# Kernel optimization log

Measured on AMD Instinct MI355X. Metric: run time of the kernel, lower is better.

The kernel has to match this reference:

```python
import jax, jax.numpy as jnp
import numpy as np

N_NODES = 100000
EPS = 1e-5


def gcn_conv(x, edge_index, W, b):
    # PyG GCNConv: add self loops, symmetric normalization, aggregate at target.
    n = x.shape[0]
    xw = x @ W                                  # [N, F_out]
    loop = jnp.arange(n)
    src = jnp.concatenate([edge_index[0], loop])
    dst = jnp.concatenate([edge_index[1], loop])
    deg = jax.ops.segment_sum(jnp.ones_like(dst, dtype=xw.dtype), dst, num_segments=n)
    dinv = jnp.where(deg > 0, jax.lax.rsqrt(deg), 0.0)
    norm = dinv[src] * dinv[dst]                # [E+N]
    out = jax.ops.segment_sum(norm[:, None] * xw[src], dst, num_segments=n)
    return out + b


def batch_norm(x, gamma, beta):
    # training-mode BatchNorm1d over node dim
    m = x.mean(axis=0)
    v = x.var(axis=0)
    return (x - m) * jax.lax.rsqrt(v + EPS) * gamma + beta


def setup_inputs() -> dict:
    key = jax.random.key(0)
    ks = jax.random.split(key, 16)
    dims = [(128, 256), (256, 128), (128, 64)]
    inp = {
        "x": jax.random.normal(ks[0], (N_NODES, 128), dtype=jnp.float32),
        "edge_index": jax.random.randint(ks[1], (2, 1600000), 0, N_NODES),
        "pos_edge_index": jax.random.randint(ks[2], (2, 200000), 0, N_NODES),
        "neg_edge_index": jax.random.randint(ks[3], (2, 200000), 0, N_NODES),
    }
    for i, (fi, fo) in enumerate(dims, start=1):
        inp[f"W{i}"] = jax.random.normal(ks[3 + i], (fi, fo), dtype=jnp.float32) / np.sqrt(fi)
        inp[f"b{i}"] = jnp.zeros((fo,), dtype=jnp.float32)
        inp[f"g{i}"] = jnp.ones((fo,), dtype=jnp.float32)
        inp[f"beta{i}"] = jnp.zeros((fo,), dtype=jnp.float32)
    return inp


def reference(x, edge_index, pos_edge_index, neg_edge_index,
              W1, b1, g1, beta1, W2, b2, g2, beta2, W3, b3, g3, beta3):
    # encode
    h = gcn_conv(x, edge_index, W1, b1)
    h = jax.nn.sigmoid(batch_norm(h, g1, beta1))
    h = gcn_conv(h, edge_index, W2, b2)
    h = jax.nn.sigmoid(batch_norm(h, g2, beta2))
    h = gcn_conv(h, edge_index, W3, b3)
    z = batch_norm(h, g3, beta3)                # [N, 64]
    # decode
    ei = jnp.concatenate([pos_edge_index, neg_edge_index], axis=-1)
    logits = jnp.sum(z[ei[0]] * z[ei[1]], axis=-1)
    return logits
```

## Files before the change

### kernel.cpp

```cpp
#include <hip/hip_runtime.h>
#include <hip/hip_bf16.h>
#include <stddef.h>


#define WAVE 64
#define BSHIFT 9
#define SCHUNK 4096

typedef __attribute__((ext_vector_type(8))) short short8;
typedef __attribute__((ext_vector_type(4))) float f32x4;

__device__ __forceinline__ float bl(uint g) { return __uint_as_float(g << 16); }
__device__ __forceinline__ float bh(uint g) { return __uint_as_float(g & 0xffff0000u); }
__device__ __forceinline__ ushort f2b(float f) {
    uint u = __float_as_uint(f);
    return (ushort)((u + 0x7fffu + ((u >> 16) & 1u)) >> 16);
}
__device__ __forceinline__ uint pack2(float lo, float hi) {
    return (uint)f2b(lo) | ((uint)f2b(hi) << 16);
}

__device__ __forceinline__ void gload16(const ushort* g, ushort* l) {
    __builtin_amdgcn_global_load_lds(
        (const __attribute__((address_space(1))) uint*)g,
        (__attribute__((address_space(3))) uint*)l, 16, 0, 0);
}

__global__ __launch_bounds__(256) void k_bhist(const int* __restrict__ dst, int* __restrict__ gh, int E) {
    __shared__ int lh[256];
    lh[threadIdx.x] = 0; __syncthreads();
    int i = blockIdx.x * 256 + threadIdx.x, stride = gridDim.x * 256;
    for (; i < E; i += stride) atomicAdd(&lh[dst[i] >> BSHIFT], 1);
    __syncthreads();
    int v = lh[threadIdx.x];
    if (v) atomicAdd(&gh[threadIdx.x], v);
}

__global__ void k_bscan(const int* __restrict__ gh, int* __restrict__ boff, int* __restrict__ bcur) {
    __shared__ int ls[256];
    int t = threadIdx.x;
    int v = gh[t];
    ls[t] = v; __syncthreads();
    for (int off = 1; off < 256; off <<= 1) {
        int x = (t >= off) ? ls[t - off] : 0;
        __syncthreads();
        ls[t] += x;
        __syncthreads();
    }
    int excl = ls[t] - v;
    boff[t] = excl; bcur[t] = excl;
    if (t == 255) boff[256] = ls[255];
}

__global__ __launch_bounds__(256) void k_bscatter(const int* __restrict__ src, const int* __restrict__ dst,
                                                  int* __restrict__ gcur, uint* __restrict__ pairs, int E) {
    __shared__ int lh[256];
    int t = threadIdx.x;
    int base = blockIdx.x * SCHUNK;
    lh[t] = 0; __syncthreads();
    int rs[16], rd[16];
    #pragma unroll
    for (int i = 0; i < 16; ++i) {
        int idx = base + i * 256 + t;
        if (idx < E) { rs[i] = src[idx]; rd[i] = dst[idx]; atomicAdd(&lh[rd[i] >> BSHIFT], 1); }
        else rd[i] = -1;
    }
    __syncthreads();
    int cnt_b = lh[t];
    int b0 = cnt_b ? atomicAdd(&gcur[t], cnt_b) : 0;
    lh[t] = b0;
    __syncthreads();
    #pragma unroll
    for (int i = 0; i < 16; ++i) {
        if (rd[i] >= 0) {
            int p = atomicAdd(&lh[rd[i] >> BSHIFT], 1);
            pairs[p] = ((uint)(rd[i] & 511) << 17) | (uint)rs[i];
        }
    }
}

__global__ __launch_bounds__(256) void k_bfine(const uint* __restrict__ pairs, const int* __restrict__ boff,
                                               int* __restrict__ rowptr, int* __restrict__ srcs,
                                               float* __restrict__ dinv, int N, int E) {
    __shared__ int lcnt[512];
    __shared__ int ls[256];
    int b = blockIdx.x, t = threadIdx.x;
    int d0 = b << BSHIFT;
    int e0 = boff[b], e1 = boff[b + 1];
    lcnt[t] = 0; lcnt[t + 256] = 0;
    __syncthreads();
    for (int e = e0 + t; e < e1; e += 256)
        atomicAdd(&lcnt[pairs[e] >> 17], 1);
    __syncthreads();
    int c0 = lcnt[2 * t], c1 = lcnt[2 * t + 1];
    ls[t] = c0 + c1;
    __syncthreads();
    for (int off = 1; off < 256; off <<= 1) {
        int x = (t >= off) ? ls[t - off] : 0;
        __syncthreads();
        ls[t] += x;
        __syncthreads();
    }
    int excl = ls[t] - (c0 + c1);
    int s0 = excl, s1 = excl + c0;
    int d = d0 + 2 * t;
    if (d < N)     { rowptr[d] = e0 + s0;     dinv[d] = rsqrtf((float)(c0 + 1)); }
    if (d + 1 < N) { rowptr[d + 1] = e0 + s1; dinv[d + 1] = rsqrtf((float)(c1 + 1)); }
    if (b == 0 && t == 0) rowptr[N] = E;
    lcnt[2 * t] = s0; lcnt[2 * t + 1] = s1;
    __syncthreads();
    for (int e = e0 + t; e < e1; e += 256) {
        uint p = pairs[e];
        int pos = atomicAdd(&lcnt[p >> 17], 1);
        srcs[e0 + pos] = (int)(p & 0x1FFFFu);
    }
}

__global__ void k_convx(const float* __restrict__ in, ushort* __restrict__ out, size_t n4) {
    size_t i = (size_t)blockIdx.x * blockDim.x + threadIdx.x;
    if (i >= n4) return;
    float4 v = reinterpret_cast<const float4*>(in)[i];
    uint2 o;
    o.x = pack2(v.x, v.y);
    o.y = pack2(v.z, v.w);
    reinterpret_cast<uint2*>(out)[i] = o;
}

__global__ void k_convW(const float* __restrict__ W1, const float* __restrict__ W2,
                        const float* __restrict__ W3, ushort* __restrict__ Wt1,
                        ushort* __restrict__ Wt2, ushort* __restrict__ Wt3) {
    int i = blockIdx.x * blockDim.x + threadIdx.x;
    const float* W; ushort* Wt; int K, Nn, j;
    if (i < 32768)      { W = W1; Wt = Wt1; K = 128; Nn = 256; j = i; }
    else if (i < 65536) { W = W2; Wt = Wt2; K = 256; Nn = 128; j = i - 32768; }
    else if (i < 73728) { W = W3; Wt = Wt3; K = 128; Nn = 64;  j = i - 65536; }
    else return;
    int k = j / Nn, n = j % Nn;
    Wt[(size_t)n * K + k] = f2b(W[k * Nn + n]);
}

template<int F>
__global__ __launch_bounds__(256) void k_agg(const ushort* __restrict__ in, ushort* __restrict__ out,
                                             const int* __restrict__ rowptr, const int* __restrict__ srcs,
                                             const float* __restrict__ dinv, int N) {
    constexpr int L = (F * 2) / 16;
    int wv = threadIdx.x >> 6, lane = threadIdx.x & 63;
    int node = (blockIdx.x * 4 + wv) * (64 / L) + lane / L;
    int sl = lane % L;
    if (node >= N) return;
    const uint4* inq = reinterpret_cast<const uint4*>(in);
    float di = dinv[node];
    float acc[8];
    {
        uint4 v = inq[(size_t)node * L + sl];
        acc[0] = di * bl(v.x); acc[1] = di * bh(v.x);
        acc[2] = di * bl(v.y); acc[3] = di * bh(v.y);
        acc[4] = di * bl(v.z); acc[5] = di * bh(v.z);
        acc[6] = di * bl(v.w); acc[7] = di * bh(v.w);
    }
    int e = rowptr[node], e1 = rowptr[node + 1];
    for (; e + 3 < e1; e += 4) {
        int s0 = srcs[e], s1 = srcs[e + 1], s2 = srcs[e + 2], s3 = srcs[e + 3];
        float d0 = dinv[s0], d1 = dinv[s1], d2 = dinv[s2], d3 = dinv[s3];
        uint4 v0 = inq[(size_t)s0 * L + sl];
        uint4 v1 = inq[(size_t)s1 * L + sl];
        uint4 v2 = inq[(size_t)s2 * L + sl];
        uint4 v3 = inq[(size_t)s3 * L + sl];
        acc[0] += d0 * bl(v0.x) + d1 * bl(v1.x) + d2 * bl(v2.x) + d3 * bl(v3.x);
        acc[1] += d0 * bh(v0.x) + d1 * bh(v1.x) + d2 * bh(v2.x) + d3 * bh(v3.x);
        acc[2] += d0 * bl(v0.y) + d1 * bl(v1.y) + d2 * bl(v2.y) + d3 * bl(v3.y);
        acc[3] += d0 * bh(v0.y) + d1 * bh(v1.y) + d2 * bh(v2.y) + d3 * bh(v3.y);
        acc[4] += d0 * bl(v0.z) + d1 * bl(v1.z) + d2 * bl(v2.z) + d3 * bl(v3.z);
        acc[5] += d0 * bh(v0.z) + d1 * bh(v1.z) + d2 * bh(v2.z) + d3 * bh(v3.z);
        acc[6] += d0 * bl(v0.w) + d1 * bl(v1.w) + d2 * bl(v2.w) + d3 * bl(v3.w);
        acc[7] += d0 * bh(v0.w) + d1 * bh(v1.w) + d2 * bh(v2.w) + d3 * bh(v3.w);
    }
    for (; e < e1; ++e) {
        int s0 = srcs[e];
        float d0 = dinv[s0];
        uint4 v0 = inq[(size_t)s0 * L + sl];
        acc[0] += d0 * bl(v0.x); acc[1] += d0 * bh(v0.x);
        acc[2] += d0 * bl(v0.y); acc[3] += d0 * bh(v0.y);
        acc[4] += d0 * bl(v0.z); acc[5] += d0 * bh(v0.z);
        acc[6] += d0 * bl(v0.w); acc[7] += d0 * bh(v0.w);
    }
    uint4 o;
    o.x = pack2(acc[0] * di, acc[1] * di);
    o.y = pack2(acc[2] * di, acc[3] * di);
    o.z = pack2(acc[4] * di, acc[5] * di);
    o.w = pack2(acc[6] * di, acc[7] * di);
    reinterpret_cast<uint4*>(out)[(size_t)node * L + sl] = o;
}

template<int F>
__global__ __launch_bounds__(256) void k_bnstats(const ushort* __restrict__ h, float* __restrict__ gsum,
                                                 float* __restrict__ gsq, int N) {
    constexpr int C = F / 8;
    constexpr int RPW = 64 / C;
    __shared__ float ls[4][16][16];
    int wv = threadIdx.x >> 6, lane = threadIdx.x & 63;
    int fidx = lane % C, rsub = lane / C;
    int row = (blockIdx.x * 4 + wv) * RPW + rsub;
    int rstride = gridDim.x * 4 * RPW;
    const uint4* hq = reinterpret_cast<const uint4*>(h);
    float s[8] = {}, q[8] = {};
    for (int r = row; r < N; r += rstride) {
        uint4 v = hq[(size_t)r * C + fidx];
        float x;
        x = bl(v.x); s[0] += x; q[0] += x * x;
        x = bh(v.x); s[1] += x; q[1] += x * x;
        x = bl(v.y); s[2] += x; q[2] += x * x;
        x = bh(v.y); s[3] += x; q[3] += x * x;
        x = bl(v.z); s[4] += x; q[4] += x * x;
        x = bh(v.z); s[5] += x; q[5] += x * x;
        x = bl(v.w); s[6] += x; q[6] += x * x;
        x = bh(v.w); s[7] += x; q[7] += x * x;
    }
    #pragma unroll
    for (int m = C; m < 64; m <<= 1) {
        #pragma unroll
        for (int j = 0; j < 8; ++j) { s[j] += __shfl_xor(s[j], m); q[j] += __shfl_xor(q[j], m); }
    }
    if (lane < C) {
        #pragma unroll
        for (int j = 0; j < 8; ++j) { ls[wv][lane][j] = s[j]; ls[wv][lane][8 + j] = q[j]; }
    }
    __syncthreads();
    int t = threadIdx.x;
    if (t < F) {
        int ch = t / 8, j = t % 8;
        float S = 0.f, Q = 0.f;
        #pragma unroll
        for (int w = 0; w < 4; ++w) { S += ls[w][ch][j]; Q += ls[w][ch][8 + j]; }
        atomicAdd(&gsum[t], S); atomicAdd(&gsq[t], Q);
    }
}

template<int F>
__global__ __launch_bounds__(256) void k_apply(ushort* __restrict__ h,
                                               const float* __restrict__ bsum, const float* __restrict__ bsq,
                                               const float* __restrict__ bg, const float* __restrict__ bb,
                                               float invN, long NT) {
    constexpr int CPR = F / 8;
    int tid = blockIdx.x * 256 + threadIdx.x;
    int fb = (tid % CPR) * 8;
    float sc[8], sh[8];
    #pragma unroll
    for (int j = 0; j < 8; ++j) {
        float m = bsum[fb + j] * invN;
        float var = bsq[fb + j] * invN - m * m;
        float s = bg[fb + j] * rsqrtf(var + 1e-5f);
        sc[j] = s; sh[j] = bb[fb + j] - m * s;
    }
    uint4* hq = reinterpret_cast<uint4*>(h);
    long stride = (long)gridDim.x * 256;
    for (long i = tid; i < NT; i += stride) {
        uint4 v = hq[i];
        float x[8];
        x[0] = bl(v.x); x[1] = bh(v.x); x[2] = bl(v.y); x[3] = bh(v.y);
        x[4] = bl(v.z); x[5] = bh(v.z); x[6] = bl(v.w); x[7] = bh(v.w);
        #pragma unroll
        for (int j = 0; j < 8; ++j) {
            float y = x[j] * sc[j] + sh[j];
            x[j] = 1.f / (1.f + __expf(-y));
        }
        v.x = pack2(x[0], x[1]); v.y = pack2(x[2], x[3]);
        v.z = pack2(x[4], x[5]); v.w = pack2(x[6], x[7]);
        hq[i] = v;
    }
}

template<int K, int NF, int NPASS, bool STATS>
__global__ __launch_bounds__(256) void k_gemm(const ushort* __restrict__ A, const ushort* __restrict__ Wt,
                                              ushort* __restrict__ C, int M, int Nout,
                                              float* __restrict__ gsum, float* __restrict__ gsq) {
    constexpr int S = K / 64;
    constexpr int KS = K / 32;
    __shared__ ushort Alds[2][128 * 64];
    int m0 = blockIdx.x * 128;
    int t = threadIdx.x;
    int w = t >> 6, lane = t & 63;
    int wr = w >> 1, wc = w & 1;
    int rf = lane & 15, kg = lane >> 4;

    auto stage = [&](int buf, int step) {
        #pragma unroll
        for (int i = 0; i < 4; ++i) {
            int cb = (i * 4 + w) * 64;
            int chunk = cb + lane;
            int r = chunk >> 3, cs = chunk & 7;
            int c = cs ^ (r & 7);
            int gr = m0 + r; if (gr >= M) gr = M - 1;
            gload16(A + (size_t)gr * K + step * 64 + c * 8, &Alds[buf][cb * 8]);
        }
    };

    for (int pass = 0; pass < NPASS; ++pass) {
        int n0 = pass * NF * 32;
        const ushort* bp[NF];
        #pragma unroll
        for (int nf = 0; nf < NF; ++nf)
            bp[nf] = Wt + (size_t)(n0 + wc * (NF * 16) + nf * 16 + rf) * K + kg * 8;

        f32x4 acc[4][NF];
        #pragma unroll
        for (int mf = 0; mf < 4; ++mf)
            #pragma unroll
            for (int nf = 0; nf < NF; ++nf)
                acc[mf][nf] = (f32x4){0.f, 0.f, 0.f, 0.f};

        if (pass == 0) {
            stage(0, 0);
            if constexpr (S == 2) stage(1, 1);
            __syncthreads();
        }

        short8 bcur[NF];
        #pragma unroll
        for (int nf = 0; nf < NF; ++nf)
            bcur[nf] = *reinterpret_cast<const short8*>(bp[nf]);

        for (int s = 0; s < S; ++s) {
            if constexpr (S > 2) {
                if (s + 1 < S && pass == 0) stage((s + 1) & 1, s + 1);
            }
            #pragma unroll
            for (int ksl = 0; ksl < 2; ++ksl) {
                int gs = s * 2 + ksl;
                short8 bnxt[NF];
                if (gs + 1 < KS) {
                    #pragma unroll
                    for (int nf = 0; nf < NF; ++nf)
                        bnxt[nf] = *reinterpret_cast<const short8*>(bp[nf] + (gs + 1) * 32);
                }
                short8 a[4];
                #pragma unroll
                for (int mf = 0; mf < 4; ++mf) {
                    int R = wr * 64 + mf * 16 + rf;
                    int idx = R * 8 + ((ksl * 4 + kg) ^ (R & 7));
                    a[mf] = *reinterpret_cast<const short8*>(&Alds[s & 1][idx * 8]);
                }
                #pragma unroll
                for (int mf = 0; mf < 4; ++mf)
                    #pragma unroll
                    for (int nf = 0; nf < NF; ++nf)
                        acc[mf][nf] = __builtin_amdgcn_mfma_f32_16x16x32_bf16(a[mf], bcur[nf], acc[mf][nf], 0, 0, 0);
                if (gs + 1 < KS) {
                    #pragma unroll
                    for (int nf = 0; nf < NF; ++nf) bcur[nf] = bnxt[nf];
                }
            }
            if constexpr (S > 2) __syncthreads();
        }

        #pragma unroll
        for (int mf = 0; mf < 4; ++mf)
            #pragma unroll
            for (int nf = 0; nf < NF; ++nf) {
                int col = n0 + wc * (NF * 16) + nf * 16 + rf;
                #pragma unroll
                for (int j = 0; j < 4; ++j) {
                    int row = m0 + wr * 64 + mf * 16 + kg * 4 + j;
                    if (row < M) C[(size_t)row * Nout + col] = f2b(acc[mf][nf][j]);
                }
            }

        if constexpr (STATS) {
            __shared__ float bns[2][NF * 32], bnq[2][NF * 32];
            __syncthreads();
            #pragma unroll
            for (int nf = 0; nf < NF; ++nf) {
                float cs = 0.f, cq = 0.f;
                #pragma unroll
                for (int mf = 0; mf < 4; ++mf)
                    #pragma unroll
                    for (int j = 0; j < 4; ++j) {
                        int row = m0 + wr * 64 + mf * 16 + kg * 4 + j;
                        float v = (row < M) ? acc[mf][nf][j] : 0.f;
                        cs += v; cq += v * v;
                    }
                cs += __shfl_xor(cs, 16); cs += __shfl_xor(cs, 32);
                cq += __shfl_xor(cq, 16); cq += __shfl_xor(cq, 32);
                if (kg == 0) { bns[wr][wc * (NF * 16) + nf * 16 + rf] = cs; bnq[wr][wc * (NF * 16) + nf * 16 + rf] = cq; }
            }
            __syncthreads();
            if (t < NF * 32) {
                atomicAdd(&gsum[n0 + t], bns[0][t] + bns[1][t]);
                atomicAdd(&gsq[n0 + t],  bnq[0][t] + bnq[1][t]);
            }
        }
    }
}

__global__ __launch_bounds__(256) void k_decode(const ushort* __restrict__ h,
                                                const float* __restrict__ bsum, const float* __restrict__ bsq,
                                                const float* __restrict__ bg, const float* __restrict__ bb,
                                                float invN,
                                                const int* __restrict__ pos, const int* __restrict__ neg,
                                                int Pp, int Pn, float* __restrict__ out) {
    __shared__ float scl[64], shl[64];
    int t = threadIdx.x;
    if (t < 64) {
        float m = bsum[t] * invN;
        float var = bsq[t] * invN - m * m;
        float sc = bg[t] * rsqrtf(var + 1e-5f);
        scl[t] = sc; shl[t] = bb[t] - m * sc;
    }
    __syncthreads();
    int gid = blockIdx.x * 16 + (t >> 4);
    int l = t & 15;
    int P = Pp + Pn;
    if (gid >= P) return;
    int a, b;
    if (gid < Pp) { a = pos[gid]; b = pos[Pp + gid]; }
    else          { int e = gid - Pp; a = neg[e]; b = neg[Pn + e]; }
    const uint2* hu = reinterpret_cast<const uint2*>(h);
    uint2 ua = hu[(size_t)a * 16 + l];
    uint2 ub = hu[(size_t)b * 16 + l];
    int f = l * 4;
    float s0 = scl[f], s1 = scl[f + 1], s2 = scl[f + 2], s3 = scl[f + 3];
    float t0 = shl[f], t1 = shl[f + 1], t2 = shl[f + 2], t3 = shl[f + 3];
    float a0 = bl(ua.x) * s0 + t0, a1 = bh(ua.x) * s1 + t1, a2 = bl(ua.y) * s2 + t2, a3 = bh(ua.y) * s3 + t3;
    float b0 = bl(ub.x) * s0 + t0, b1 = bh(ub.x) * s1 + t1, b2 = bl(ub.y) * s2 + t2, b3 = bh(ub.y) * s3 + t3;
    float d = a0 * b0 + a1 * b1 + a2 * b2 + a3 * b3;
    d += __shfl_xor(d, 1);
    d += __shfl_xor(d, 2);
    d += __shfl_xor(d, 4);
    d += __shfl_xor(d, 8);
    if (l == 0) out[gid] = d;
}

extern "C" void kernel_launch(void* const* d_in, const int* in_sizes, int n_in,
                              void* d_out, int out_size, void* d_ws, size_t ws_size,
                              hipStream_t stream) {
    const float* x   = (const float*)d_in[0];
    const int*   ei  = (const int*)d_in[1];
    const int*   pe  = (const int*)d_in[2];
    const int*   ne  = (const int*)d_in[3];
    const float* W1  = (const float*)d_in[4];
    const float* g1  = (const float*)d_in[6];
    const float* be1 = (const float*)d_in[7];
    const float* W2  = (const float*)d_in[8];
    const float* g2  = (const float*)d_in[10];
    const float* be2 = (const float*)d_in[11];
    const float* W3  = (const float*)d_in[12];
    const float* g3  = (const float*)d_in[14];
    const float* be3 = (const float*)d_in[15];
    float* out = (float*)d_out;

    const int N  = in_sizes[0] / 128;
    const int E  = in_sizes[1] / 2;
    const int Pp = in_sizes[2] / 2;
    const int Pn = in_sizes[3] / 2;
    const float invN = 1.0f / (float)N;

    char* ws = (char*)d_ws;
    auto carve = [&](size_t bytes) -> char* {
        char* p = ws;
        ws += (bytes + 255) & ~(size_t)255;
        return p;
    };
    char*  zz     = carve(256 * 4 + 896 * 4);
    int*   gh     = (int*)zz;
    float* sums1  = (float*)(zz + 1024);
    float* sq1    = sums1 + 256;
    float* sums2  = sq1 + 256;
    float* sq2    = sums2 + 128;
    float* sums3  = sq2 + 128;
    float* sq3    = sums3 + 64;
    size_t zz_bytes = 1024 + 896 * 4;

    int*    boff   = (int*)carve(257 * 4);
    int*    bcur   = (int*)carve(256 * 4);
    int*    rowptr = (int*)carve((size_t)(N + 1) * 4);
    float*  dinv   = (float*)carve((size_t)N * 4);
    int*    srcs   = (int*)carve((size_t)E * 4);
    uint*   pairs  = (uint*)carve((size_t)E * 4);
    ushort* Wt1    = (ushort*)carve(128 * 256 * 2);
    ushort* Wt2    = (ushort*)carve(256 * 128 * 2);
    ushort* Wt3    = (ushort*)carve(128 * 64 * 2);
    ushort* b1     = (ushort*)carve((size_t)N * 128 * 2);
    ushort* b2     = (ushort*)carve((size_t)N * 128 * 2);
    ushort* b3     = (ushort*)carve((size_t)N * 256 * 2);

    const int* e_src = ei;
    const int* e_dst = ei + E;
    const int NBUCK = (N + (1 << BSHIFT) - 1) >> BSHIFT;

    hipMemsetAsync(zz, 0, zz_bytes, stream);

    k_bhist<<<2048, 256, 0, stream>>>(e_dst, gh, E);
    k_bscan<<<1, 256, 0, stream>>>(gh, boff, bcur);
    k_bscatter<<<(E + SCHUNK - 1) / SCHUNK, 256, 0, stream>>>(e_src, e_dst, bcur, pairs, E);
    k_bfine<<<NBUCK, 256, 0, stream>>>(pairs, boff, rowptr, srcs, dinv, N, E);

    {
        size_t n4 = (size_t)N * 128 / 4;
        k_convx<<<(int)((n4 + 255) / 256), 256, 0, stream>>>(x, b1, n4);
        k_convW<<<288, 256, 0, stream>>>(W1, W2, W3, Wt1, Wt2, Wt3);
    }

    const int mblk = (N + 127) / 128;
    const int agg128 = (N + 15) / 16;
    const int agg64  = (N + 31) / 32;

    k_agg<128><<<agg128, 256, 0, stream>>>(b1, b2, rowptr, srcs, dinv, N);
    k_gemm<128, 4, 2, true><<<mblk, 256, 0, stream>>>(b2, Wt1, b3, N, 256, sums1, sq1);
    k_apply<256><<<2048, 256, 0, stream>>>(b3, sums1, sq1, g1, be1, invN, (long)N * 32);

    k_gemm<256, 4, 1, false><<<mblk, 256, 0, stream>>>(b3, Wt2, b1, N, 128, nullptr, nullptr);
    k_agg<128><<<agg128, 256, 0, stream>>>(b1, b2, rowptr, srcs, dinv, N);
    k_bnstats<128><<<512, 256, 0, stream>>>(b2, sums2, sq2, N);
    k_apply<128><<<2048, 256, 0, stream>>>(b2, sums2, sq2, g2, be2, invN, (long)N * 16);

    k_gemm<128, 2, 1, false><<<mblk, 256, 0, stream>>>(b2, Wt3, b1, N, 64, nullptr, nullptr);
    k_agg<64><<<agg64, 256, 0, stream>>>(b1, b2, rowptr, srcs, dinv, N);
    k_bnstats<64><<<512, 256, 0, stream>>>(b2, sums3, sq3, N);

    k_decode<<<(Pp + Pn + 15) / 16, 256, 0, stream>>>(b2, sums3, sq3, g3, be3, invN,
                                                      pe, ne, Pp, Pn, out);
}
```

Baseline: 544.4 us.

## Prescale features by source dinv to drop per-edge dinv gathers in aggregation

The source-side normalization dinv[src] is moved out of the aggregation loop. The input features are pre-multiplied by dinv once per node, in the x conversion kernel and in the GEMM epilogues for layers 2 and 3. The aggregation kernel then sums raw neighbor rows with no per-edge dinv gather or multiply, and its main loop is unrolled to 8 loads in flight. The W and x conversion kernels are merged into one launch. The cost is an extra rounding step: the features are scaled before they are stored as bf16.

```diff
diff --git a/kernel.cpp b/kernel.cpp
--- a/kernel.cpp
+++ b/kernel.cpp
@@ -116,27 +116,29 @@
     }
 }
 
-__global__ void k_convx(const float* __restrict__ in, ushort* __restrict__ out, size_t n4) {
-    size_t i = (size_t)blockIdx.x * blockDim.x + threadIdx.x;
-    if (i >= n4) return;
-    float4 v = reinterpret_cast<const float4*>(in)[i];
+__global__ void k_conv(const float* __restrict__ W1, const float* __restrict__ W2,
+                       const float* __restrict__ W3, ushort* __restrict__ Wt1,
+                       ushort* __restrict__ Wt2, ushort* __restrict__ Wt3,
+                       const float* __restrict__ x, const float* __restrict__ dinv,
+                       ushort* __restrict__ xs, size_t n4) {
+    size_t i = (size_t)blockIdx.x * 256 + threadIdx.x;
+    if (i < 73728) {
+        const float* W; ushort* Wt; int K, Nn; size_t j;
+        if (i < 32768)      { W = W1; Wt = Wt1; K = 128; Nn = 256; j = i; }
+        else if (i < 65536) { W = W2; Wt = Wt2; K = 256; Nn = 128; j = i - 32768; }
+        else                { W = W3; Wt = Wt3; K = 128; Nn = 64;  j = i - 65536; }
+        int k = (int)(j / Nn), n = (int)(j % Nn);
+        Wt[(size_t)n * K + k] = f2b(W[(size_t)k * Nn + n]);
+        return;
+    }
+    size_t j = i - 73728;
+    if (j >= n4) return;
+    float d = dinv[j / 32];
+    float4 v = reinterpret_cast<const float4*>(x)[j];
     uint2 o;
-    o.x = pack2(v.x, v.y);
-    o.y = pack2(v.z, v.w);
-    reinterpret_cast<uint2*>(out)[i] = o;
-}
-
-__global__ void k_convW(const float* __restrict__ W1, const float* __restrict__ W2,
-                        const float* __restrict__ W3, ushort* __restrict__ Wt1,
-                        ushort* __restrict__ Wt2, ushort* __restrict__ Wt3) {
-    int i = blockIdx.x * blockDim.x + threadIdx.x;
-    const float* W; ushort* Wt; int K, Nn, j;
-    if (i < 32768)      { W = W1; Wt = Wt1; K = 128; Nn = 256; j = i; }
-    else if (i < 65536) { W = W2; Wt = Wt2; K = 256; Nn = 128; j = i - 32768; }
-    else if (i < 73728) { W = W3; Wt = Wt3; K = 128; Nn = 64;  j = i - 65536; }
-    else return;
-    int k = j / Nn, n = j % Nn;
-    Wt[(size_t)n * K + k] = f2b(W[k * Nn + n]);
+    o.x = pack2(d * v.x, d * v.y);
+    o.y = pack2(d * v.z, d * v.w);
+    reinterpret_cast<uint2*>(xs)[j] = o;
 }
 
 template<int F>
@@ -153,36 +155,48 @@
     float acc[8];
     {
         uint4 v = inq[(size_t)node * L + sl];
-        acc[0] = di * bl(v.x); acc[1] = di * bh(v.x);
-        acc[2] = di * bl(v.y); acc[3] = di * bh(v.y);
-        acc[4] = di * bl(v.z); acc[5] = di * bh(v.z);
-        acc[6] = di * bl(v.w); acc[7] = di * bh(v.w);
+        acc[0] = bl(v.x); acc[1] = bh(v.x);
+        acc[2] = bl(v.y); acc[3] = bh(v.y);
+        acc[4] = bl(v.z); acc[5] = bh(v.z);
+        acc[6] = bl(v.w); acc[7] = bh(v.w);
     }
     int e = rowptr[node], e1 = rowptr[node + 1];
+    for (; e + 7 < e1; e += 8) {
+        int s[8];
+        #pragma unroll
+        for (int i = 0; i < 8; ++i) s[i] = srcs[e + i];
+        uint4 v[8];
+        #pragma unroll
+        for (int i = 0; i < 8; ++i) v[i] = inq[(size_t)s[i] * L + sl];
+        #pragma unroll
+        for (int i = 0; i < 8; ++i) {
+            acc[0] += bl(v[i].x); acc[1] += bh(v[i].x);
+            acc[2] += bl(v[i].y); acc[3] += bh(v[i].y);
+            acc[4] += bl(v[i].z); acc[5] += bh(v[i].z);
+            acc[6] += bl(v[i].w); acc[7] += bh(v[i].w);
+        }
+    }
     for (; e + 3 < e1; e += 4) {
-        int s0 = srcs[e], s1 = srcs[e + 1], s2 = srcs[e + 2], s3 = srcs[e + 3];
-        float d0 = dinv[s0], d1 = dinv[s1], d2 = dinv[s2], d3 = dinv[s3];
-        uint4 v0 = inq[(size_t)s0 * L + sl];
-        uint4 v1 = inq[(size_t)s1 * L + sl];
-        uint4 v2 = inq[(size_t)s2 * L + sl];
-        uint4 v3 = inq[(size_t)s3 * L + sl];
-        acc[0] += d0 * bl(v0.x) + d1 * bl(v1.x) + d2 * bl(v2.x) + d3 * bl(v3.x);
-        acc[1] += d0 * bh(v0.x) + d1 * bh(v1.x) + d2 * bh(v2.x) + d3 * bh(v3.x);
-        acc[2] += d0 * bl(v0.y) + d1 * bl(v1.y) + d2 * bl(v2.y) + d3 * bl(v3.y);
-        acc[3] += d0 * bh(v0.y) + d1 * bh(v1.y) + d2 * bh(v2.y) + d3 * bh(v3.y);
-        acc[4] += d0 * bl(v0.z) + d1 * bl(v1.z) + d2 * bl(v2.z) + d3 * bl(v3.z);
-        acc[5] += d0 * bh(v0.z) + d1 * bh(v1.z) + d2 * bh(v2.z) + d3 * bh(v3.z);
-        acc[6] += d0 * bl(v0.w) + d1 * bl(v1.w) + d2 * bl(v2.w) + d3 * bl(v3.w);
-        acc[7] += d0 * bh(v0.w) + d1 * bh(v1.w) + d2 * bh(v2.w) + d3 * bh(v3.w);
+        int s[4];
+        #pragma unroll
+        for (int i = 0; i < 4; ++i) s[i] = srcs[e + i];
+        uint4 v[4];
+        #pragma unroll
+        for (int i = 0; i < 4; ++i) v[i] = inq[(size_t)s[i] * L + sl];
+        #pragma unroll
+        for (int i = 0; i < 4; ++i) {
+            acc[0] += bl(v[i].x); acc[1] += bh(v[i].x);
+            acc[2] += bl(v[i].y); acc[3] += bh(v[i].y);
+            acc[4] += bl(v[i].z); acc[5] += bh(v[i].z);
+            acc[6] += bl(v[i].w); acc[7] += bh(v[i].w);
+        }
     }
     for (; e < e1; ++e) {
-        int s0 = srcs[e];
-        float d0 = dinv[s0];
-        uint4 v0 = inq[(size_t)s0 * L + sl];
-        acc[0] += d0 * bl(v0.x); acc[1] += d0 * bh(v0.x);
-        acc[2] += d0 * bl(v0.y); acc[3] += d0 * bh(v0.y);
-        acc[4] += d0 * bl(v0.z); acc[5] += d0 * bh(v0.z);
-        acc[6] += d0 * bl(v0.w); acc[7] += d0 * bh(v0.w);
+        uint4 v0 = inq[(size_t)srcs[e] * L + sl];
+        acc[0] += bl(v0.x); acc[1] += bh(v0.x);
+        acc[2] += bl(v0.y); acc[3] += bh(v0.y);
+        acc[4] += bl(v0.z); acc[5] += bh(v0.z);
+        acc[6] += bl(v0.w); acc[7] += bh(v0.w);
     }
     uint4 o;
     o.x = pack2(acc[0] * di, acc[1] * di);
@@ -270,9 +284,10 @@
     }
 }
 
-template<int K, int NF, int NPASS, bool STATS>
+template<int K, int NF, int NPASS, bool STATS, bool PRESCALE>
 __global__ __launch_bounds__(256) void k_gemm(const ushort* __restrict__ A, const ushort* __restrict__ Wt,
                                               ushort* __restrict__ C, int M, int Nout,
+                                              const float* __restrict__ dinv,
                                               float* __restrict__ gsum, float* __restrict__ gsq) {
     constexpr int S = K / 64;
     constexpr int KS = K / 32;
@@ -294,6 +309,17 @@
             gload16(A + (size_t)gr * K + step * 64 + c * 8, &Alds[buf][cb * 8]);
         }
     };
+
+    float dreg[4][4];
+    if constexpr (PRESCALE) {
+        #pragma unroll
+        for (int mf = 0; mf < 4; ++mf)
+            #pragma unroll
+            for (int j = 0; j < 4; ++j) {
+                int row = m0 + wr * 64 + mf * 16 + kg * 4 + j;
+                dreg[mf][j] = (row < M) ? dinv[row] : 0.f;
+            }
+    }
 
     for (int pass = 0; pass < NPASS; ++pass) {
         int n0 = pass * NF * 32;
@@ -361,7 +387,9 @@
                 #pragma unroll
                 for (int j = 0; j < 4; ++j) {
                     int row = m0 + wr * 64 + mf * 16 + kg * 4 + j;
-                    if (row < M) C[(size_t)row * Nout + col] = f2b(acc[mf][nf][j]);
+                    float v = acc[mf][nf][j];
+                    if constexpr (PRESCALE) v *= dreg[mf][j];
+                    if (row < M) C[(size_t)row * Nout + col] = f2b(v);
                 }
             }
 
@@ -496,8 +524,8 @@
 
     {
         size_t n4 = (size_t)N * 128 / 4;
-        k_convx<<<(int)((n4 + 255) / 256), 256, 0, stream>>>(x, b1, n4);
-        k_convW<<<288, 256, 0, stream>>>(W1, W2, W3, Wt1, Wt2, Wt3);
+        int blocks = (int)((73728 + n4 + 255) / 256);
+        k_conv<<<blocks, 256, 0, stream>>>(W1, W2, W3, Wt1, Wt2, Wt3, x, dinv, b1, n4);
     }
 
     const int mblk = (N + 127) / 128;
@@ -505,15 +533,15 @@
     const int agg64  = (N + 31) / 32;
 
     k_agg<128><<<agg128, 256, 0, stream>>>(b1, b2, rowptr, srcs, dinv, N);
-    k_gemm<128, 4, 2, true><<<mblk, 256, 0, stream>>>(b2, Wt1, b3, N, 256, sums1, sq1);
+    k_gemm<128, 4, 2, true, false><<<mblk, 256, 0, stream>>>(b2, Wt1, b3, N, 256, nullptr, sums1, sq1);
     k_apply<256><<<2048, 256, 0, stream>>>(b3, sums1, sq1, g1, be1, invN, (long)N * 32);
 
-    k_gemm<256, 4, 1, false><<<mblk, 256, 0, stream>>>(b3, Wt2, b1, N, 128, nullptr, nullptr);
+    k_gemm<256, 4, 1, false, true><<<mblk, 256, 0, stream>>>(b3, Wt2, b1, N, 128, dinv, nullptr, nullptr);
     k_agg<128><<<agg128, 256, 0, stream>>>(b1, b2, rowptr, srcs, dinv, N);
     k_bnstats<128><<<512, 256, 0, stream>>>(b2, sums2, sq2, N);
     k_apply<128><<<2048, 256, 0, stream>>>(b2, sums2, sq2, g2, be2, invN, (long)N * 16);
 
-    k_gemm<128, 2, 1, false><<<mblk, 256, 0, stream>>>(b2, Wt3, b1, N, 64, nullptr, nullptr);
+    k_gemm<128, 2, 1, false, true><<<mblk, 256, 0, stream>>>(b2, Wt3, b1, N, 64, dinv, nullptr, nullptr);
     k_agg<64><<<agg64, 256, 0, stream>>>(b1, b2, rowptr, srcs, dinv, N);
     k_bnstats<64><<<512, 256, 0, stream>>>(b2, sums3, sq3, N);
 
```

Measured after the change: 536.6 us. About the same (-1.4%).
